# Kernel tuning notes

Measured on AMD Instinct MI355X. Metric: run time of the kernel, lower is better.

Reference implementation:

```python
import jax, jax.numpy as jnp
import numpy as np

REGION = 64  # region_size r

def setup_inputs() -> dict:
    key = jax.random.key(0)
    B, C, H, W, k, r, T = 16, 64, 256, 256, 3, REGION, 32
    k0, k1, k2, k3, k4 = jax.random.split(key, 5)
    x = jax.random.normal(k0, (B, C, H, W), dtype=jnp.float32)
    weight = jax.random.normal(k1, (C, C, k, k), dtype=jnp.float32) * 0.05  # [out,in,kh,kw]
    h_idx = jax.random.randint(k2, (T,), 0, H - r + 1, dtype=jnp.int32)
    w_idx = jax.random.randint(k3, (T,), 0, W - r + 1, dtype=jnp.int32)
    lambdas = jax.random.uniform(k4, (T,), dtype=jnp.float32)
    return {"x": x, "weight": weight, "h_idx": h_idx, "w_idx": w_idx, "lambdas": lambdas}

def reference(x, weight, h_idx, w_idx, lambdas):
    B, C, H, W = x.shape
    k = weight.shape[-1]
    r = REGION
    n_r = (H // r) * (W // r)
    out_r = r - k + 1  # conv 'VALID' output size per region

    def step(out, t):
        h, w, lam = t
        crop = jax.lax.dynamic_slice(x, (0, 0, h, w), (B, C, r, r))
        c = jax.lax.conv_general_dilated(
            crop, weight, window_strides=(1, 1), padding='VALID',
            dimension_numbers=('NCHW', 'OIHW', 'NCHW'))
        cur = jax.lax.dynamic_slice(out, (0, 0, h, w), (B, C, out_r, out_r))
        out = jax.lax.dynamic_update_slice(out, cur + lam * c, (0, 0, h, w))
        return out, None

    out, _ = jax.lax.scan(step, jnp.zeros_like(x), (h_idx, w_idx, lambdas))
    return out / n_r
```

## Files before the change

### kernel.cpp

```cpp
#include <hip/hip_runtime.h>


typedef short short8 __attribute__((ext_vector_type(8)));
typedef float floatx4 __attribute__((ext_vector_type(4)));
typedef unsigned int uint4v __attribute__((ext_vector_type(4)));

#define OUTR 62

__device__ inline unsigned f2bf_pack(float lo, float hi) {
    unsigned ul = __builtin_bit_cast(unsigned, lo);
    unsigned uh = __builtin_bit_cast(unsigned, hi);
    ul = (ul + 0x7FFFu + ((ul >> 16) & 1u)) >> 16;
    uh = (uh + 0x7FFFu + ((uh >> 16) & 1u)) >> 16;
    return ul | (uh << 16);
}

__global__ void srconv_coeff_kernel(const int* __restrict__ h_idx,
                                    const int* __restrict__ w_idx,
                                    const float* __restrict__ lam,
                                    int T, float* __restrict__ coeff) {
    int p = blockIdx.x;
    int q = threadIdx.x;
    float c = 0.f;
    for (int t = 0; t < T; ++t) {
        int dh = p - h_idx[t];
        int dw = q - w_idx[t];
        if (dh >= 0 && dh < OUTR && dw >= 0 && dw < OUTR) c += lam[t];
    }
    coeff[(p << 8) + q] = c * (1.0f / 16.0f);
}

__global__ void srconv_wtrans_kernel(const float* __restrict__ wgt,
                                     uint4v* __restrict__ afrag) {
    int id = blockIdx.x * 256 + threadIdx.x;
    int l  = id & 63;
    int fi = id >> 6;
    int m  = fi & 3;
    int cb = (fi >> 2) & 1;
    int kk = fi >> 3;
    int co  = m * 16 + (l & 15);
    int ci0 = cb * 32 + (l >> 4) * 8;
    float w[8];
#pragma unroll
    for (int j = 0; j < 8; ++j)
        w[j] = wgt[(co * 64 + ci0 + j) * 9 + kk];
    uint4v d;
    d.x = f2bf_pack(w[0], w[1]);
    d.y = f2bf_pack(w[2], w[3]);
    d.z = f2bf_pack(w[4], w[5]);
    d.w = f2bf_pack(w[6], w[7]);
    afrag[id] = d;
}

__launch_bounds__(256, 3)
__global__ void srconv_fused_kernel(const float* __restrict__ x,
                                    const float* __restrict__ coeff,
                                    const short8* __restrict__ afrag,
                                    float* __restrict__ out) {
    __shared__ __align__(16) unsigned xs[340 * 16];

    const int tid  = threadIdx.x;
    const int lane = tid & 63;
    const int wv   = tid >> 6;
    const int l15  = lane & 15;
    const int kg   = lane >> 4;

    const unsigned bid = blockIdx.x;
    const unsigned swz = (bid & 7) * 512 + (bid >> 3);
    const int b    = swz >> 8;
    const int tile = swz & 255;
    const int P0   = (tile >> 3) << 3;
    const int Q0   = (tile & 7) << 5;

    float myc = coeff[((P0 + (tid >> 5)) << 8) + Q0 + (tid & 31)];
    if (__syncthreads_count(myc != 0.f) == 0) {
        const floatx4 z = (floatx4){0.f, 0.f, 0.f, 0.f};
        for (int u = tid; u < 64 * 8 * 8; u += 256) {
            int q4 = u & 7;
            int pr = (u >> 3) & 7;
            int co = u >> 6;
            *(floatx4*)(out + (((b << 6) + co) << 16) +
                        ((P0 + pr) << 8) + Q0 + (q4 << 2)) = z;
        }
        return;
    }

    floatx4 acc[4][2][2];
#pragma unroll
    for (int m = 0; m < 4; ++m)
#pragma unroll
        for (int p = 0; p < 2; ++p)
#pragma unroll
            for (int h = 0; h < 2; ++h)
                acc[m][p][h] = (floatx4){0.f, 0.f, 0.f, 0.f};

    const float* xb  = x + ((size_t)b << 22);
    const int    prb = P0 + (wv << 1);

    for (int cb = 0; cb < 2; ++cb) {
        if (cb) __syncthreads();
#pragma unroll
        for (int r = 0; r < 6; ++r) {
            int u  = r * 256 + tid;
            int uc = u < 1440 ? u : 1439;
            int cp    = uc / 90;
            int rem   = uc - cp * 90;
            int row   = rem / 9;
            int chunk = rem - row * 9;
            int gr    = min(P0 + row, 255);
            int gcb   = min(Q0 + (chunk << 2), 252);
            const float* xp = xb + (((cb << 4) + cp) << 17) + (gr << 8) + gcb;
            const floatx4 v0 = *(const floatx4*)(xp);
            const floatx4 v1 = *(const floatx4*)(xp + 65536);
            const int c4   = chunk << 2;
#pragma unroll
            for (int j = 0; j < 4; ++j) {
                if (u < 1440 && c4 + j < 34) {
                    int pix = row * 34 + c4 + j;
                    int slot = cp ^ (((pix >> 1) & 3) << 2);
                    xs[(pix << 4) + slot] = f2bf_pack(v0[j], v1[j]);
                }
            }
        }
        __syncthreads();

        const short8* af = afrag + (cb << 8);
        short8 a_cur[4];
#pragma unroll
        for (int m = 0; m < 4; ++m)
            a_cur[m] = af[(m << 6) + lane];
#pragma unroll
        for (int kk = 0; kk < 9; ++kk) {
            const int kh = kk / 3;
            const int kw = kk - kh * 3;
            short8 a_nxt[4];
            if (kk < 8) {
                const short8* afn = af + ((kk + 1) << 9);
#pragma unroll
                for (int m = 0; m < 4; ++m)
                    a_nxt[m] = afn[(m << 6) + lane];
            }
            short8 bf[2][2];
#pragma unroll
            for (int p = 0; p < 2; ++p)
#pragma unroll
                for (int h = 0; h < 2; ++h) {
                    int prl = (wv << 1) + p + kh;
                    int cl  = (h << 4) + l15 + kw;
                    int pix = prl * 34 + cl;
                    int off = (pix << 4) +
                              ((kg << 2) ^ (((pix >> 1) & 3) << 2));
                    bf[p][h] = *(const short8*)(&xs[off]);
                }
#pragma unroll
            for (int m = 0; m < 4; ++m)
#pragma unroll
                for (int p = 0; p < 2; ++p)
#pragma unroll
                    for (int h = 0; h < 2; ++h)
                        acc[m][p][h] = __builtin_amdgcn_mfma_f32_16x16x32_bf16(
                            a_cur[m], bf[p][h], acc[m][p][h], 0, 0, 0);
            if (kk < 8) {
#pragma unroll
                for (int m = 0; m < 4; ++m) a_cur[m] = a_nxt[m];
            }
        }
    }
    __syncthreads();

    float cf[2][2];
#pragma unroll
    for (int p = 0; p < 2; ++p)
#pragma unroll
        for (int h = 0; h < 2; ++h)
            cf[p][h] = coeff[((prb + p) << 8) + Q0 + (h << 4) + l15];

    float* epb = reinterpret_cast<float*>(xs);
    const int co_l = lane >> 3;
    const int q4   = lane & 7;

#pragma unroll
    for (int p = 0; p < 2; ++p) {
        const int pr = prb + p;
#pragma unroll
        for (int m = 0; m < 4; ++m) {
            float* ep = epb + (((wv << 1) + (m & 1)) * 576);
#pragma unroll
            for (int h = 0; h < 2; ++h)
#pragma unroll
                for (int reg = 0; reg < 4; ++reg)
                    ep[((kg << 2) + reg) * 36 + (h << 4) + l15] =
                        acc[m][p][h][reg] * cf[p][h];
#pragma unroll
            for (int j = 0; j < 2; ++j) {
                const floatx4 v = *reinterpret_cast<const floatx4*>(
                    &ep[(co_l + (j << 3)) * 36 + (q4 << 2)]);
                const int co = (m << 4) + co_l + (j << 3);
                *(floatx4*)(out + (((b << 6) + co) << 16) +
                            (pr << 8) + Q0 + (q4 << 2)) = v;
            }
        }
    }
}

extern "C" void kernel_launch(void* const* d_in, const int* in_sizes, int n_in,
                              void* d_out, int out_size, void* d_ws, size_t ws_size,
                              hipStream_t stream) {
    const float* x     = (const float*)d_in[0];
    const float* wgt   = (const float*)d_in[1];
    const int*   h_idx = (const int*)d_in[2];
    const int*   w_idx = (const int*)d_in[3];
    const float* lam   = (const float*)d_in[4];
    float*       out   = (float*)d_out;
    float*       coeff = (float*)d_ws;
    char*        af_b  = (char*)d_ws + 65536 * sizeof(float);
    const int    T     = in_sizes[2];

    srconv_coeff_kernel<<<256, 256, 0, stream>>>(h_idx, w_idx, lam, T, coeff);
    srconv_wtrans_kernel<<<18, 256, 0, stream>>>(wgt, (uint4v*)af_b);
    srconv_fused_kernel<<<4096, 256, 0, stream>>>(
        x, coeff, (const short8*)af_b, out);
}
```

Baseline: 210.3 us.

## Stage all 32 channel pairs in LDS at once and double-buffer weight fragments

Shared memory grows to hold both channel halves, so the input tile for all 64 channels is loaded in one pass with a single barrier, replacing two load/compute phases. The 18 kernel-tap/channel-block steps are fully unrolled and the weight fragments are prefetched two steps ahead from global memory. The coefficient loads are hoisted before the main loop. Doubling LDS to about 43KB per block may reduce how many blocks fit per CU, and it removes the overlap that two phases allowed between one half's loads and the other half's compute.

```diff
diff --git a/kernel.cpp b/kernel.cpp
--- a/kernel.cpp
+++ b/kernel.cpp
@@ -57,7 +57,7 @@
                                     const float* __restrict__ coeff,
                                     const short8* __restrict__ afrag,
                                     float* __restrict__ out) {
-    __shared__ __align__(16) unsigned xs[340 * 16];
+    __shared__ __align__(16) unsigned xs[2 * 340 * 16];
 
     const int tid  = threadIdx.x;
     const int lane = tid & 63;
@@ -85,6 +85,44 @@
         return;
     }
 
+    const int prb = P0 + (wv << 1);
+
+    float cf[2][2];
+#pragma unroll
+    for (int p = 0; p < 2; ++p)
+#pragma unroll
+        for (int h = 0; h < 2; ++h)
+            cf[p][h] = coeff[((prb + p) << 8) + Q0 + (h << 4) + l15];
+
+    const float* xb = x + ((size_t)b << 22);
+
+#pragma unroll
+    for (int r = 0; r < 12; ++r) {
+        int u  = r * 256 + tid;
+        int uc = u < 2880 ? u : 2879;
+        int cp    = uc / 90;
+        int rem   = uc - cp * 90;
+        int row   = rem / 9;
+        int chunk = rem - row * 9;
+        int gr    = min(P0 + row, 255);
+        int gcb   = min(Q0 + (chunk << 2), 252);
+        const float* xp = xb + (cp << 17) + (gr << 8) + gcb;
+        const floatx4 v0 = *(const floatx4*)(xp);
+        const floatx4 v1 = *(const floatx4*)(xp + 65536);
+        const int c4  = chunk << 2;
+        const int cbo = (cp >> 4) * 5440;
+        const int cpl = cp & 15;
+#pragma unroll
+        for (int j = 0; j < 4; ++j) {
+            if (u < 2880 && c4 + j < 34) {
+                int pix = row * 34 + c4 + j;
+                int slot = cpl ^ (((pix >> 1) & 3) << 2);
+                xs[cbo + (pix << 4) + slot] = f2bf_pack(v0[j], v1[j]);
+            }
+        }
+    }
+    __syncthreads();
+
     floatx4 acc[4][2][2];
 #pragma unroll
     for (int m = 0; m < 4; ++m)
@@ -94,86 +132,53 @@
             for (int h = 0; h < 2; ++h)
                 acc[m][p][h] = (floatx4){0.f, 0.f, 0.f, 0.f};
 
-    const float* xb  = x + ((size_t)b << 22);
-    const int    prb = P0 + (wv << 1);
-
-    for (int cb = 0; cb < 2; ++cb) {
-        if (cb) __syncthreads();
-#pragma unroll
-        for (int r = 0; r < 6; ++r) {
-            int u  = r * 256 + tid;
-            int uc = u < 1440 ? u : 1439;
-            int cp    = uc / 90;
-            int rem   = uc - cp * 90;
-            int row   = rem / 9;
-            int chunk = rem - row * 9;
-            int gr    = min(P0 + row, 255);
-            int gcb   = min(Q0 + (chunk << 2), 252);
-            const float* xp = xb + (((cb << 4) + cp) << 17) + (gr << 8) + gcb;
-            const floatx4 v0 = *(const floatx4*)(xp);
-            const floatx4 v1 = *(const floatx4*)(xp + 65536);
-            const int c4   = chunk << 2;
-#pragma unroll
-            for (int j = 0; j < 4; ++j) {
-                if (u < 1440 && c4 + j < 34) {
-                    int pix = row * 34 + c4 + j;
-                    int slot = cp ^ (((pix >> 1) & 3) << 2);
-                    xs[(pix << 4) + slot] = f2bf_pack(v0[j], v1[j]);
-                }
+    short8 areg[2][4];
+#pragma unroll
+    for (int m = 0; m < 4; ++m) {
+        areg[0][m] = afrag[((0 * 2 + 0) * 4 + m) * 64 + lane];
+        areg[1][m] = afrag[((1 * 2 + 0) * 4 + m) * 64 + lane];
+    }
+
+#pragma unroll
+    for (int t = 0; t < 18; ++t) {
+        const int cb = t / 9;
+        const int kk = t - cb * 9;
+        const int kh = kk / 3;
+        const int kw = kk - kh * 3;
+        const int cur = t & 1;
+
+        short8 bf[2][2];
+#pragma unroll
+        for (int p = 0; p < 2; ++p)
+#pragma unroll
+            for (int h = 0; h < 2; ++h) {
+                int prl = (wv << 1) + p + kh;
+                int cl  = (h << 4) + l15 + kw;
+                int pix = prl * 34 + cl;
+                int off = cb * 5440 + (pix << 4) +
+                          ((kg << 2) ^ (((pix >> 1) & 3) << 2));
+                bf[p][h] = *(const short8*)(&xs[off]);
             }
-        }
-        __syncthreads();
-
-        const short8* af = afrag + (cb << 8);
-        short8 a_cur[4];
 #pragma unroll
         for (int m = 0; m < 4; ++m)
-            a_cur[m] = af[(m << 6) + lane];
-#pragma unroll
-        for (int kk = 0; kk < 9; ++kk) {
-            const int kh = kk / 3;
-            const int kw = kk - kh * 3;
-            short8 a_nxt[4];
-            if (kk < 8) {
-                const short8* afn = af + ((kk + 1) << 9);
-#pragma unroll
-                for (int m = 0; m < 4; ++m)
-                    a_nxt[m] = afn[(m << 6) + lane];
-            }
-            short8 bf[2][2];
 #pragma unroll
             for (int p = 0; p < 2; ++p)
 #pragma unroll
-                for (int h = 0; h < 2; ++h) {
-                    int prl = (wv << 1) + p + kh;
-                    int cl  = (h << 4) + l15 + kw;
-                    int pix = prl * 34 + cl;
-                    int off = (pix << 4) +
-                              ((kg << 2) ^ (((pix >> 1) & 3) << 2));
-                    bf[p][h] = *(const short8*)(&xs[off]);
-                }
+                for (int h = 0; h < 2; ++h)
+                    acc[m][p][h] = __builtin_amdgcn_mfma_f32_16x16x32_bf16(
+                        areg[cur][m], bf[p][h], acc[m][p][h], 0, 0, 0);
+
+        if (t < 16) {
+            const int tn  = t + 2;
+            const int cbn = tn / 9;
+            const int kkn = tn - cbn * 9;
 #pragma unroll
             for (int m = 0; m < 4; ++m)
-#pragma unroll
-                for (int p = 0; p < 2; ++p)
-#pragma unroll
-                    for (int h = 0; h < 2; ++h)
-                        acc[m][p][h] = __builtin_amdgcn_mfma_f32_16x16x32_bf16(
-                            a_cur[m], bf[p][h], acc[m][p][h], 0, 0, 0);
-            if (kk < 8) {
-#pragma unroll
-                for (int m = 0; m < 4; ++m) a_cur[m] = a_nxt[m];
-            }
+                areg[cur][m] =
+                    afrag[(((kkn << 1) + cbn) * 4 + m) * 64 + lane];
         }
     }
     __syncthreads();
-
-    float cf[2][2];
-#pragma unroll
-    for (int p = 0; p < 2; ++p)
-#pragma unroll
-        for (int h = 0; h < 2; ++h)
-            cf[p][h] = coeff[((prb + p) << 8) + Q0 + (h << 4) + l15];
 
     float* epb = reinterpret_cast<float*>(xs);
     const int co_l = lane >> 3;
```

New measurement: 191.9 us. 8.8% less time.
